# Kernel tuning notes

Measured on AMD Instinct MI355X. Metric: run time of the kernel, lower is better.

Reference implementation:

```python
import jax, jax.numpy as jnp
import numpy as np

N_NODES = 50000
N_EDGES = 800000
D = 128          # node_state_dim
H = 256          # edge hidden / message dim (= 2*D)
NH = 256         # node MLP hidden


def setup_inputs() -> dict:
    key = jax.random.key(0)
    ks = jax.random.split(key, 20)
    s = 0.05
    inp = {
        "node_states": jax.random.normal(ks[0], (N_NODES, D), jnp.float32),
        "edge_features": jax.random.normal(ks[1], (N_EDGES, 1), jnp.float32),
        "from_idx": jax.random.randint(ks[2], (N_EDGES,), 0, N_NODES, jnp.int32),
        "to_idx": jax.random.randint(ks[3], (N_EDGES,), 0, N_NODES, jnp.int32),
        # forward-direction message net: Linear(2D+1 -> H), ReLU, Linear(H -> H)
        "W1": jax.random.normal(ks[4], (2 * D + 1, H), jnp.float32) * s,
        "b1": jnp.zeros((H,), jnp.float32),
        "W2": jax.random.normal(ks[5], (H, H), jnp.float32) * s,
        "b2": jnp.zeros((H,), jnp.float32),
        # reverse-direction message net (separate params)
        "RW1": jax.random.normal(ks[6], (2 * D + 1, H), jnp.float32) * s,
        "Rb1": jnp.zeros((H,), jnp.float32),
        "RW2": jax.random.normal(ks[7], (H, H), jnp.float32) * s,
        "Rb2": jnp.zeros((H,), jnp.float32),
        # node update MLP: Linear(3D -> NH), ReLU, Linear(NH -> D)
        "Wn1": jax.random.normal(ks[8], (3 * D, NH), jnp.float32) * s,
        "bn1": jnp.zeros((NH,), jnp.float32),
        "Wn2": jax.random.normal(ks[9], (NH, D), jnp.float32) * s,
        "bn2": jnp.zeros((D,), jnp.float32),
    }
    return inp


def _mlp2(x, W1, b1, W2, b2):
    return jax.nn.relu(x @ W1 + b1) @ W2 + b2


def reference(node_states, edge_features, from_idx, to_idx,
              W1, b1, W2, b2, RW1, Rb1, RW2, Rb2, Wn1, bn1, Wn2, bn2):
    n_nodes = node_states.shape[0]
    from_states = node_states[from_idx]            # [E, D]
    to_states = node_states[to_idx]                # [E, D]

    # forward direction: messages go to to_idx
    edge_in = jnp.concatenate([from_states, to_states, edge_features], axis=-1)  # [E, 2D+1]
    msgs = _mlp2(edge_in, W1, b1, W2, b2)                                        # [E, H]
    agg = jax.ops.segment_sum(msgs, to_idx, num_segments=n_nodes)                # [N, H]

    # reverse direction: swap roles, aggregate onto from_idx
    redge_in = jnp.concatenate([to_states, from_states, edge_features], axis=-1)
    rmsgs = _mlp2(redge_in, RW1, Rb1, RW2, Rb2)
    agg = agg + jax.ops.segment_sum(rmsgs, from_idx, num_segments=n_nodes)

    # residual node update: MLP on [agg, node_states] -> [N, D]
    upd_in = jnp.concatenate([agg, node_states], axis=-1)                        # [N, 3D]
    return node_states + _mlp2(upd_in, Wn1, bn1, Wn2, bn2)
```

## Files before the change

### kernel.cpp

```cpp
#include <hip/hip_runtime.h>
#include <hip/hip_bf16.h>


typedef __bf16 bf16;
typedef __attribute__((ext_vector_type(8))) __bf16 bf16x8;
typedef __attribute__((ext_vector_type(4))) __bf16 bf16x4v;
typedef __attribute__((ext_vector_type(4))) float floatx4;
typedef __attribute__((ext_vector_type(2))) float floatx2;

#define DD 128
#define HH 256
#define CAPB 1408
#define MAXBINS 1600

__device__ __forceinline__ bf16x8 ns8(const float* __restrict__ NS, int row, int col, int N) {
    bf16x8 v;
    if (row < N) {
        float4 f0 = *(const float4*)&NS[(size_t)row * DD + col];
        float4 f1 = *(const float4*)&NS[(size_t)row * DD + col + 4];
        v[0] = (bf16)f0.x; v[1] = (bf16)f0.y; v[2] = (bf16)f0.z; v[3] = (bf16)f0.w;
        v[4] = (bf16)f1.x; v[5] = (bf16)f1.y; v[6] = (bf16)f1.z; v[7] = (bf16)f1.w;
    } else {
        v = (bf16x8)(bf16)0.0f;
    }
    return v;
}

__global__ void k_prep(const float* __restrict__ W1, const float* __restrict__ RW1,
                       const float* __restrict__ W2, const float* __restrict__ RW2,
                       const float* __restrict__ Wn1, const float* __restrict__ Wn2,
                       const float* __restrict__ b2, const float* __restrict__ Rb2,
                       bf16* __restrict__ Wt1, bf16* __restrict__ Wth,
                       bf16* __restrict__ Wt2, float* __restrict__ u,
                       float* __restrict__ ru) {
    const int b = blockIdx.x, t = threadIdx.x;
    if (b < 512) {
        int idx = b * 256 + t;
        int n = idx >> 7, k = idx & 127;
        float v;
        if (n < 256)      v = W1[k * 256 + n];
        else if (n < 512) v = W1[(128 + k) * 256 + (n - 256)];
        else if (n < 768) v = RW1[k * 256 + (n - 512)];
        else              v = RW1[(128 + k) * 256 + (n - 768)];
        Wt1[idx] = (bf16)v;
    } else if (b < 1152) {
        int k = b - 512, m = t;
        float v;
        if (k < 512) {
            const float* Wsrc = (k < 256) ? W2 : RW2;
            int i = k & 255;
            float acc = 0.f;
            for (int j = 0; j < 256; ++j) acc += Wsrc[i * 256 + j] * Wn1[j * 256 + m];
            v = acc;
        } else {
            v = Wn1[(256 + k - 512) * 256 + m];
        }
        Wth[m * 640 + k] = (bf16)v;
    } else if (b < 1280) {
        int idx = (b - 1152) * 256 + t;
        int n = idx >> 8, k = idx & 255;
        Wt2[idx] = (bf16)Wn2[k * 128 + n];
    } else {
        int m = t;
        float a = 0.f, bb = 0.f;
        for (int j = 0; j < 256; ++j) {
            float w = Wn1[j * 256 + m];
            a += b2[j] * w;
            bb += Rb2[j] * w;
        }
        u[m] = a;
        ru[m] = bb;
    }
}

__global__ __launch_bounds__(256) void k_bins(
    const int* __restrict__ from_idx, const int* __restrict__ to_idx,
    const float* __restrict__ ef, int* __restrict__ gcur,
    int2* __restrict__ binbuf, int E, int NP, int NBINS) {
    __shared__ int hist[MAXBINS];
    __shared__ int base[MAXBINS];
    const int t = threadIdx.x;
    const int NBF = NP >> 6;
    for (int i = t; i < NBINS; i += 256) hist[i] = 0;
    __syncthreads();
    const int e0 = blockIdx.x * 2048;
    int f[8], tt[8]; float w[8]; bool valid[8];
#pragma unroll
    for (int q = 0; q < 8; ++q) {
        int e = e0 + q * 256 + t;
        valid[q] = e < E;
        int ec = valid[q] ? e : 0;
        f[q] = from_idx[ec]; tt[q] = to_idx[ec]; w[q] = ef[ec];
    }
#pragma unroll
    for (int q = 0; q < 8; ++q) {
        if (valid[q]) {
            atomicAdd(&hist[tt[q] >> 6], 1);
            atomicAdd(&hist[NBF + (f[q] >> 6)], 1);
        }
    }
    __syncthreads();
    for (int i = t; i < NBINS; i += 256) {
        int h = hist[i];
        base[i] = h ? atomicAdd(&gcur[i], h) : 0;
        hist[i] = 0;
    }
    __syncthreads();
#pragma unroll
    for (int q = 0; q < 8; ++q) {
        if (valid[q]) {
            int wb = __float_as_int(w[q]);
            int b1 = tt[q] >> 6;
            int r1 = base[b1] + atomicAdd(&hist[b1], 1);
            if (r1 < CAPB)
                binbuf[(size_t)b1 * CAPB + r1] = make_int2(((tt[q] & 63) << 17) | f[q], wb);
            int b2 = NBF + (f[q] >> 6);
            int r2 = base[b2] + atomicAdd(&hist[b2], 1);
            if (r2 < CAPB)
                binbuf[(size_t)b2 * CAPB + r2] = make_int2(((f[q] & 63) << 17) | tt[q], wb);
        }
    }
}

__global__ __launch_bounds__(256) void k_proj(const float* __restrict__ NS,
                                              const bf16* __restrict__ Wt,
                                              unsigned char* __restrict__ Pn,
                                              bf16* __restrict__ Pf, int N) {
    __shared__ __align__(16) bf16 As[2][64][40];
    __shared__ __align__(16) bf16 Bs[2][64][40];
    const int tid = threadIdx.x;
    const int wv = tid >> 6, lane = tid & 63;
    const int l15 = lane & 15, quad = lane >> 4;
    const int row0 = blockIdx.y * 64, col0 = blockIdx.x * 64;
    const int srow = tid >> 2, kc = (tid & 3) * 8;
    floatx4 acc[4] = {};
    for (int k0 = 0; k0 < DD; k0 += 64) {
        bf16x8 av0 = ns8(NS, row0 + srow, k0 + kc, N);
        bf16x8 av1 = ns8(NS, row0 + srow, k0 + 32 + kc, N);
        bf16x8 bv0 = *(const bf16x8*)&Wt[(size_t)(col0 + srow) * DD + k0 + kc];
        bf16x8 bv1 = *(const bf16x8*)&Wt[(size_t)(col0 + srow) * DD + k0 + 32 + kc];
        __syncthreads();
        *(bf16x8*)&As[0][srow][kc] = av0;
        *(bf16x8*)&As[1][srow][kc] = av1;
        *(bf16x8*)&Bs[0][srow][kc] = bv0;
        *(bf16x8*)&Bs[1][srow][kc] = bv1;
        __syncthreads();
#pragma unroll
        for (int h = 0; h < 2; ++h) {
            bf16x8 bfr = *(const bf16x8*)&Bs[h][wv * 16 + l15][quad * 8];
#pragma unroll
            for (int r = 0; r < 4; ++r) {
                bf16x8 afr = *(const bf16x8*)&As[h][r * 16 + l15][quad * 8];
                acc[r] = __builtin_amdgcn_mfma_f32_16x16x32_bf16(afr, bfr, acc[r], 0, 0, 0);
            }
        }
    }
    const int ocol = col0 + wv * 16 + l15;
    const int ch = ocol & 255;
    const int half = (ocol >> 9) & 1;
    const bool isNbr = ((ocol >> 8) & 1) == 0;
#pragma unroll
    for (int r = 0; r < 4; ++r)
#pragma unroll
        for (int i = 0; i < 4; ++i) {
            int orow = row0 + r * 16 + quad * 4 + i;
            float v = acc[r][i];
            if (isNbr) {
                int pk = __builtin_amdgcn_cvt_pk_fp8_f32(v, v, 0, false);
                Pn[(size_t)orow * 512 + half * 256 + ch] = (unsigned char)(pk & 0xFF);
            } else {
                Pf[(size_t)orow * 512 + half * 256 + ch] = (bf16)v;
            }
        }
}

__global__ __launch_bounds__(256) void k_aggf(
    const unsigned char* __restrict__ Pn, const bf16* __restrict__ Pf,
    const int2* __restrict__ binbuf, const int* __restrict__ gcnt,
    const float* __restrict__ W1, const float* __restrict__ b1,
    const float* __restrict__ RW1, const float* __restrict__ Rb1,
    bf16* __restrict__ S_to, bf16* __restrict__ S_fr,
    int* __restrict__ deg, int NP) {
    __shared__ int hist[64], kstart[64], cur[64], scanbuf[64];
    __shared__ int2 srec[CAPB];
    const int b = blockIdx.x, t = threadIdx.x;
    const int NBF = NP >> 6;
    const bool rev = b >= NBF;
    const int node0 = (rev ? b - NBF : b) << 6;
    int cnt = gcnt[b]; if (cnt > CAPB) cnt = CAPB;
    const int2* bin = binbuf + (size_t)b * CAPB;
    if (t < 64) hist[t] = 0;
    __syncthreads();
    for (int i = t; i < cnt; i += 256)
        atomicAdd(&hist[((unsigned)bin[i].x) >> 17], 1);
    __syncthreads();
    if (t < 64) scanbuf[t] = hist[t];
    __syncthreads();
    for (int d = 1; d < 64; d <<= 1) {
        int v = (t < 64 && t >= d) ? scanbuf[t - d] : 0;
        __syncthreads();
        if (t < 64) scanbuf[t] += v;
        __syncthreads();
    }
    if (t < 64) { kstart[t] = scanbuf[t] - hist[t]; cur[t] = scanbuf[t] - hist[t]; }
    __syncthreads();
    for (int i = t; i < cnt; i += 256) {
        int2 r = bin[i];
        int rk = atomicAdd(&cur[((unsigned)r.x) >> 17], 1);
        srec[rk] = r;
    }
    __syncthreads();
    const int wv = t >> 6, lane = t & 63, c = lane * 4;
    const int fixoff = rev ? 256 : 0;
    const int nbroff = rev ? 256 : 0;
    const float* bb = rev ? Rb1 : b1;
    const float* wl = (rev ? RW1 : W1) + 65536;
    float4 bv = *(const float4*)&bb[c];
    float4 wv4 = *(const float4*)&wl[c];
    bf16* Sarr = rev ? S_fr : S_to;
    for (int key = wv; key < 64; key += 4) {
        int node = node0 + key;
        bf16x4v pf = *(const bf16x4v*)&Pf[(size_t)node * 512 + fixoff + c];
        float fx0 = (float)pf[0] + bv.x;
        float fx1 = (float)pf[1] + bv.y;
        float fx2 = (float)pf[2] + bv.z;
        float fx3 = (float)pf[3] + bv.w;
        int beg = kstart[key], kc2 = hist[key], end = beg + kc2;
        float a0 = 0.f, a1 = 0.f, a2 = 0.f, a3 = 0.f;
        int j = beg;
        for (; j + 4 <= end; j += 4) {
            int2 r0 = srec[j], r1 = srec[j + 1], r2 = srec[j + 2], r3 = srec[j + 3];
            int q0 = *(const int*)&Pn[(size_t)(r0.x & 0x1FFFF) * 512 + nbroff + c];
            int q1 = *(const int*)&Pn[(size_t)(r1.x & 0x1FFFF) * 512 + nbroff + c];
            int q2 = *(const int*)&Pn[(size_t)(r2.x & 0x1FFFF) * 512 + nbroff + c];
            int q3 = *(const int*)&Pn[(size_t)(r3.x & 0x1FFFF) * 512 + nbroff + c];
#pragma unroll
            for (int z = 0; z < 4; ++z) {
                int qq = z == 0 ? q0 : z == 1 ? q1 : z == 2 ? q2 : q3;
                float w = __int_as_float(z == 0 ? r0.y : z == 1 ? r1.y : z == 2 ? r2.y : r3.y);
                floatx2 lo = __builtin_amdgcn_cvt_pk_f32_fp8(qq, false);
                floatx2 hi = __builtin_amdgcn_cvt_pk_f32_fp8(qq, true);
                a0 += fmaxf(fx0 + lo.x + w * wv4.x, 0.f);
                a1 += fmaxf(fx1 + lo.y + w * wv4.y, 0.f);
                a2 += fmaxf(fx2 + hi.x + w * wv4.z, 0.f);
                a3 += fmaxf(fx3 + hi.y + w * wv4.w, 0.f);
            }
        }
        for (; j < end; ++j) {
            int2 r = srec[j];
            int qq = *(const int*)&Pn[(size_t)(r.x & 0x1FFFF) * 512 + nbroff + c];
            float w = __int_as_float(r.y);
            floatx2 lo = __builtin_amdgcn_cvt_pk_f32_fp8(qq, false);
            floatx2 hi = __builtin_amdgcn_cvt_pk_f32_fp8(qq, true);
            a0 += fmaxf(fx0 + lo.x + w * wv4.x, 0.f);
            a1 += fmaxf(fx1 + lo.y + w * wv4.y, 0.f);
            a2 += fmaxf(fx2 + hi.x + w * wv4.z, 0.f);
            a3 += fmaxf(fx3 + hi.y + w * wv4.w, 0.f);
        }
        bf16x4v o;
        o[0] = (bf16)a0; o[1] = (bf16)a1; o[2] = (bf16)a2; o[3] = (bf16)a3;
        *(bf16x4v*)&Sarr[(size_t)node * 256 + c] = o;
        if (lane == 0) deg[(rev ? NP : 0) + node] = kc2;
    }
}

__global__ __launch_bounds__(256) void k_node(
    const bf16* __restrict__ S_to, const bf16* __restrict__ S_fr,
    const float* __restrict__ NS, const bf16* __restrict__ Wth,
    const bf16* __restrict__ Wt2,
    const float* __restrict__ u, const float* __restrict__ ru,
    const float* __restrict__ bn1, const float* __restrict__ bn2,
    const int* __restrict__ deg, float* __restrict__ out, int NP, int N) {
    __shared__ __align__(16) unsigned char smem[33792];
    bf16 (*As)[40]  = (bf16(*)[40])smem;
    bf16 (*Bs)[40]  = (bf16(*)[40])(smem + 5120);
    bf16 (*Hs)[264] = (bf16(*)[264])smem;
    const int tid = threadIdx.x;
    const int wv = tid >> 6, lane = tid & 63;
    const int l15 = lane & 15, quad = lane >> 4;
    const int row0 = blockIdx.x * 64;
    const int srow = tid >> 2, kc = (tid & 3) * 8;
    floatx4 acc[4][4] = {};
    const int arow = row0 + srow;
    for (int k0 = 0; k0 < 640; k0 += 32) {
        bf16x8 av;
        if (k0 < 512) {
            const bf16* S = (k0 < 256) ? S_to : S_fr;
            av = *(const bf16x8*)&S[(size_t)arow * 256 + (k0 & 255) + kc];
        } else {
            av = ns8(NS, arow, (k0 - 512) + kc, N);
        }
        bf16x8 bv[4];
#pragma unroll
        for (int j = 0; j < 4; ++j)
            bv[j] = *(const bf16x8*)&Wth[(size_t)(srow + 64 * j) * 640 + k0 + kc];
        __syncthreads();
        *(bf16x8*)&As[srow][kc] = av;
#pragma unroll
        for (int j = 0; j < 4; ++j)
            *(bf16x8*)&Bs[srow + 64 * j][kc] = bv[j];
        __syncthreads();
#pragma unroll
        for (int s = 0; s < 4; ++s) {
            bf16x8 bfr = *(const bf16x8*)&Bs[wv * 64 + s * 16 + l15][quad * 8];
#pragma unroll
            for (int r = 0; r < 4; ++r) {
                bf16x8 afr = *(const bf16x8*)&As[r * 16 + l15][quad * 8];
                acc[s][r] = __builtin_amdgcn_mfma_f32_16x16x32_bf16(afr, bfr, acc[s][r], 0, 0, 0);
            }
        }
    }
    __syncthreads();
#pragma unroll
    for (int s = 0; s < 4; ++s) {
        int col = wv * 64 + s * 16 + l15;
        float uc = u[col], rc = ru[col], bc = bn1[col];
#pragma unroll
        for (int r = 0; r < 4; ++r)
#pragma unroll
            for (int i = 0; i < 4; ++i) {
                int row = r * 16 + quad * 4 + i;
                float v = acc[s][r][i] + (float)deg[row0 + row] * uc
                        + (float)deg[NP + row0 + row] * rc + bc;
                Hs[row][col] = (bf16)fmaxf(v, 0.f);
            }
    }
    __syncthreads();
    floatx4 acc2[2][4] = {};
    for (int k0 = 0; k0 < HH; k0 += 32) {
        bf16x8 afr[4];
#pragma unroll
        for (int r = 0; r < 4; ++r)
            afr[r] = *(const bf16x8*)&Hs[r * 16 + l15][k0 + quad * 8];
#pragma unroll
        for (int s = 0; s < 2; ++s) {
            int col = wv * 32 + s * 16 + l15;
            bf16x8 bfr = *(const bf16x8*)&Wt2[(size_t)col * HH + k0 + quad * 8];
#pragma unroll
            for (int r = 0; r < 4; ++r)
                acc2[s][r] = __builtin_amdgcn_mfma_f32_16x16x32_bf16(afr[r], bfr, acc2[s][r], 0, 0, 0);
        }
    }
#pragma unroll
    for (int s = 0; s < 2; ++s) {
        int ocol = wv * 32 + s * 16 + l15;
        float bb = bn2[ocol];
#pragma unroll
        for (int r = 0; r < 4; ++r)
#pragma unroll
            for (int i = 0; i < 4; ++i) {
                int orow = row0 + r * 16 + quad * 4 + i;
                if (orow < N)
                    out[(size_t)orow * DD + ocol] = acc2[s][r][i] + bb + NS[(size_t)orow * DD + ocol];
            }
    }
}

extern "C" void kernel_launch(void* const* d_in, const int* in_sizes, int n_in,
                              void* d_out, int out_size, void* d_ws, size_t ws_size,
                              hipStream_t stream) {
    const float* NS   = (const float*)d_in[0];
    const float* ef   = (const float*)d_in[1];
    const int* from_idx = (const int*)d_in[2];
    const int* to_idx   = (const int*)d_in[3];
    const float* W1  = (const float*)d_in[4];
    const float* b1  = (const float*)d_in[5];
    const float* W2  = (const float*)d_in[6];
    const float* b2  = (const float*)d_in[7];
    const float* RW1 = (const float*)d_in[8];
    const float* Rb1 = (const float*)d_in[9];
    const float* RW2 = (const float*)d_in[10];
    const float* Rb2 = (const float*)d_in[11];
    const float* Wn1 = (const float*)d_in[12];
    const float* bn1 = (const float*)d_in[13];
    const float* Wn2 = (const float*)d_in[14];
    const float* bn2 = (const float*)d_in[15];

    const int N  = in_sizes[0] / DD;
    const int E  = in_sizes[2];
    const int NP = ((N + 63) / 64) * 64;
    const int MB = NP / 64;
    const int NBF = NP / 64;
    const int NBINS = 2 * NBF;

    char* base = (char*)d_ws;
    size_t off_b = 0;
    auto alloc = [&](size_t b) { size_t o = off_b; off_b += (b + 255) & ~(size_t)255; return o; };
    unsigned char* Pn = (unsigned char*)(base + alloc((size_t)NP * 512));
    bf16* Pf   = (bf16*)(base + alloc((size_t)NP * 512 * 2));
    bf16* S_to = (bf16*)(base + alloc((size_t)NP * 256 * 2));
    bf16* S_fr = (bf16*)(base + alloc((size_t)NP * 256 * 2));
    int* deg   = (int*)(base + alloc((size_t)2 * NP * 4));
    int* gcur  = (int*)(base + alloc((size_t)NBINS * 4));
    int2* binbuf = (int2*)(base + alloc((size_t)NBINS * CAPB * 8));
    bf16* Wt1 = (bf16*)(base + alloc(1024 * 128 * 2));
    bf16* Wth = (bf16*)(base + alloc(256 * 640 * 2));
    bf16* Wt2 = (bf16*)(base + alloc(128 * 256 * 2));
    float* u  = (float*)(base + alloc(256 * 4));
    float* ru = (float*)(base + alloc(256 * 4));

    hipMemsetAsync(gcur, 0, (size_t)NBINS * 4, stream);

    k_prep<<<1281, 256, 0, stream>>>(W1, RW1, W2, RW2, Wn1, Wn2, b2, Rb2,
                                     Wt1, Wth, Wt2, u, ru);

    k_bins<<<(E + 2047) / 2048, 256, 0, stream>>>(from_idx, to_idx, ef, gcur,
                                                  binbuf, E, NP, NBINS);

    k_proj<<<dim3(16, MB), 256, 0, stream>>>(NS, Wt1, Pn, Pf, N);
    k_aggf<<<NBINS, 256, 0, stream>>>(Pn, Pf, binbuf, gcur, W1, b1, RW1, Rb1,
                                      S_to, S_fr, deg, NP);
    k_node<<<MB, 256, 0, stream>>>(S_to, S_fr, NS, Wth, Wt2, u, ru, bn1, bn2,
                                   deg, (float*)d_out, NP, N);
}
```

Baseline: 343.0 us.

## Merge prep, binning and projection into one front kernel; deepen aggregation and node loops

Three independent kernels (weight prep, edge binning, node projection) become one launch that splits by block index. The projection now reads W1/RW1 directly from fp32 and converts them in shared memory, so the transposed Wt1 buffer is gone. The aggregation gather loop is unrolled from 4 to 8 records to keep more loads in flight. The node kernel loads 64-wide K chunks (two halves) per barrier pair instead of 32, halving barrier count at the cost of more shared memory (51 KB), which may reduce occupancy.

New measurement: 346.1 us. About the same (+0.9%).

```diff
diff --git a/kernel.cpp b/kernel.cpp
--- a/kernel.cpp
+++ b/kernel.cpp
@@ -26,152 +26,158 @@
     return v;
 }
 
-__global__ void k_prep(const float* __restrict__ W1, const float* __restrict__ RW1,
-                       const float* __restrict__ W2, const float* __restrict__ RW2,
-                       const float* __restrict__ Wn1, const float* __restrict__ Wn2,
-                       const float* __restrict__ b2, const float* __restrict__ Rb2,
-                       bf16* __restrict__ Wt1, bf16* __restrict__ Wth,
-                       bf16* __restrict__ Wt2, float* __restrict__ u,
-                       float* __restrict__ ru) {
+__global__ __launch_bounds__(256) void k_front(
+    const float* __restrict__ NS, const int* __restrict__ from_idx,
+    const int* __restrict__ to_idx, const float* __restrict__ ef,
+    const float* __restrict__ W1, const float* __restrict__ RW1,
+    const float* __restrict__ W2, const float* __restrict__ RW2,
+    const float* __restrict__ Wn1, const float* __restrict__ Wn2,
+    const float* __restrict__ b2, const float* __restrict__ Rb2,
+    int* __restrict__ gcur, int2* __restrict__ binbuf,
+    unsigned char* __restrict__ Pn, bf16* __restrict__ Pf,
+    bf16* __restrict__ Wth, bf16* __restrict__ Wt2,
+    float* __restrict__ u, float* __restrict__ ru,
+    int E, int N, int NP, int NBINS, int BINB, int MB) {
+    __shared__ __align__(16) unsigned char smem[20608];
     const int b = blockIdx.x, t = threadIdx.x;
-    if (b < 512) {
-        int idx = b * 256 + t;
-        int n = idx >> 7, k = idx & 127;
-        float v;
-        if (n < 256)      v = W1[k * 256 + n];
-        else if (n < 512) v = W1[(128 + k) * 256 + (n - 256)];
-        else if (n < 768) v = RW1[k * 256 + (n - 512)];
-        else              v = RW1[(128 + k) * 256 + (n - 768)];
-        Wt1[idx] = (bf16)v;
-    } else if (b < 1152) {
-        int k = b - 512, m = t;
-        float v;
-        if (k < 512) {
-            const float* Wsrc = (k < 256) ? W2 : RW2;
-            int i = k & 255;
-            float acc = 0.f;
-            for (int j = 0; j < 256; ++j) acc += Wsrc[i * 256 + j] * Wn1[j * 256 + m];
-            v = acc;
+
+    if (b < BINB) {
+        int* hist = (int*)smem;
+        int* base = hist + MAXBINS;
+        const int NBF = NP >> 6;
+        for (int i = t; i < NBINS; i += 256) hist[i] = 0;
+        __syncthreads();
+        const int e0 = b * 2048;
+        int f[8], tt[8]; float w[8]; bool valid[8];
+#pragma unroll
+        for (int q = 0; q < 8; ++q) {
+            int e = e0 + q * 256 + t;
+            valid[q] = e < E;
+            int ec = valid[q] ? e : 0;
+            f[q] = from_idx[ec]; tt[q] = to_idx[ec]; w[q] = ef[ec];
+        }
+#pragma unroll
+        for (int q = 0; q < 8; ++q) {
+            if (valid[q]) {
+                atomicAdd(&hist[tt[q] >> 6], 1);
+                atomicAdd(&hist[NBF + (f[q] >> 6)], 1);
+            }
+        }
+        __syncthreads();
+        for (int i = t; i < NBINS; i += 256) {
+            int h = hist[i];
+            base[i] = h ? atomicAdd(&gcur[i], h) : 0;
+            hist[i] = 0;
+        }
+        __syncthreads();
+#pragma unroll
+        for (int q = 0; q < 8; ++q) {
+            if (valid[q]) {
+                int wb = __float_as_int(w[q]);
+                int b1 = tt[q] >> 6;
+                int r1 = base[b1] + atomicAdd(&hist[b1], 1);
+                if (r1 < CAPB)
+                    binbuf[(size_t)b1 * CAPB + r1] = make_int2(((tt[q] & 63) << 17) | f[q], wb);
+                int b2i = NBF + (f[q] >> 6);
+                int r2 = base[b2i] + atomicAdd(&hist[b2i], 1);
+                if (r2 < CAPB)
+                    binbuf[(size_t)b2i * CAPB + r2] = make_int2(((f[q] & 63) << 17) | tt[q], wb);
+            }
+        }
+        return;
+    }
+
+    if (b < BINB + 769) {
+        int bb = b - BINB;
+        if (bb < 640) {
+            int k = bb, m = t;
+            float v;
+            if (k < 512) {
+                const float* Wsrc = (k < 256) ? W2 : RW2;
+                int i = k & 255;
+                float acc = 0.f;
+                for (int j = 0; j < 256; ++j) acc += Wsrc[i * 256 + j] * Wn1[j * 256 + m];
+                v = acc;
+            } else {
+                v = Wn1[(256 + k - 512) * 256 + m];
+            }
+            Wth[m * 640 + k] = (bf16)v;
+        } else if (bb < 768) {
+            int idx = (bb - 640) * 256 + t;
+            int n = idx >> 8, k = idx & 255;
+            Wt2[idx] = (bf16)Wn2[k * 128 + n];
         } else {
-            v = Wn1[(256 + k - 512) * 256 + m];
-        }
-        Wth[m * 640 + k] = (bf16)v;
-    } else if (b < 1280) {
-        int idx = (b - 1152) * 256 + t;
-        int n = idx >> 8, k = idx & 255;
-        Wt2[idx] = (bf16)Wn2[k * 128 + n];
-    } else {
-        int m = t;
-        float a = 0.f, bb = 0.f;
-        for (int j = 0; j < 256; ++j) {
-            float w = Wn1[j * 256 + m];
-            a += b2[j] * w;
-            bb += Rb2[j] * w;
-        }
-        u[m] = a;
-        ru[m] = bb;
-    }
-}
-
-__global__ __launch_bounds__(256) void k_bins(
-    const int* __restrict__ from_idx, const int* __restrict__ to_idx,
-    const float* __restrict__ ef, int* __restrict__ gcur,
-    int2* __restrict__ binbuf, int E, int NP, int NBINS) {
-    __shared__ int hist[MAXBINS];
-    __shared__ int base[MAXBINS];
-    const int t = threadIdx.x;
-    const int NBF = NP >> 6;
-    for (int i = t; i < NBINS; i += 256) hist[i] = 0;
-    __syncthreads();
-    const int e0 = blockIdx.x * 2048;
-    int f[8], tt[8]; float w[8]; bool valid[8];
-#pragma unroll
-    for (int q = 0; q < 8; ++q) {
-        int e = e0 + q * 256 + t;
-        valid[q] = e < E;
-        int ec = valid[q] ? e : 0;
-        f[q] = from_idx[ec]; tt[q] = to_idx[ec]; w[q] = ef[ec];
-    }
-#pragma unroll
-    for (int q = 0; q < 8; ++q) {
-        if (valid[q]) {
-            atomicAdd(&hist[tt[q] >> 6], 1);
-            atomicAdd(&hist[NBF + (f[q] >> 6)], 1);
-        }
-    }
-    __syncthreads();
-    for (int i = t; i < NBINS; i += 256) {
-        int h = hist[i];
-        base[i] = h ? atomicAdd(&gcur[i], h) : 0;
-        hist[i] = 0;
-    }
-    __syncthreads();
-#pragma unroll
-    for (int q = 0; q < 8; ++q) {
-        if (valid[q]) {
-            int wb = __float_as_int(w[q]);
-            int b1 = tt[q] >> 6;
-            int r1 = base[b1] + atomicAdd(&hist[b1], 1);
-            if (r1 < CAPB)
-                binbuf[(size_t)b1 * CAPB + r1] = make_int2(((tt[q] & 63) << 17) | f[q], wb);
-            int b2 = NBF + (f[q] >> 6);
-            int r2 = base[b2] + atomicAdd(&hist[b2], 1);
-            if (r2 < CAPB)
-                binbuf[(size_t)b2 * CAPB + r2] = make_int2(((f[q] & 63) << 17) | tt[q], wb);
-        }
-    }
-}
-
-__global__ __launch_bounds__(256) void k_proj(const float* __restrict__ NS,
-                                              const bf16* __restrict__ Wt,
-                                              unsigned char* __restrict__ Pn,
-                                              bf16* __restrict__ Pf, int N) {
-    __shared__ __align__(16) bf16 As[2][64][40];
-    __shared__ __align__(16) bf16 Bs[2][64][40];
-    const int tid = threadIdx.x;
-    const int wv = tid >> 6, lane = tid & 63;
-    const int l15 = lane & 15, quad = lane >> 4;
-    const int row0 = blockIdx.y * 64, col0 = blockIdx.x * 64;
-    const int srow = tid >> 2, kc = (tid & 3) * 8;
-    floatx4 acc[4] = {};
-    for (int k0 = 0; k0 < DD; k0 += 64) {
-        bf16x8 av0 = ns8(NS, row0 + srow, k0 + kc, N);
-        bf16x8 av1 = ns8(NS, row0 + srow, k0 + 32 + kc, N);
-        bf16x8 bv0 = *(const bf16x8*)&Wt[(size_t)(col0 + srow) * DD + k0 + kc];
-        bf16x8 bv1 = *(const bf16x8*)&Wt[(size_t)(col0 + srow) * DD + k0 + 32 + kc];
-        __syncthreads();
-        *(bf16x8*)&As[0][srow][kc] = av0;
-        *(bf16x8*)&As[1][srow][kc] = av1;
-        *(bf16x8*)&Bs[0][srow][kc] = bv0;
-        *(bf16x8*)&Bs[1][srow][kc] = bv1;
-        __syncthreads();
-#pragma unroll
-        for (int h = 0; h < 2; ++h) {
-            bf16x8 bfr = *(const bf16x8*)&Bs[h][wv * 16 + l15][quad * 8];
-#pragma unroll
-            for (int r = 0; r < 4; ++r) {
-                bf16x8 afr = *(const bf16x8*)&As[h][r * 16 + l15][quad * 8];
-                acc[r] = __builtin_amdgcn_mfma_f32_16x16x32_bf16(afr, bfr, acc[r], 0, 0, 0);
-            }
-        }
-    }
-    const int ocol = col0 + wv * 16 + l15;
-    const int ch = ocol & 255;
-    const int half = (ocol >> 9) & 1;
-    const bool isNbr = ((ocol >> 8) & 1) == 0;
-#pragma unroll
-    for (int r = 0; r < 4; ++r)
-#pragma unroll
-        for (int i = 0; i < 4; ++i) {
-            int orow = row0 + r * 16 + quad * 4 + i;
-            float v = acc[r][i];
-            if (isNbr) {
-                int pk = __builtin_amdgcn_cvt_pk_fp8_f32(v, v, 0, false);
-                Pn[(size_t)orow * 512 + half * 256 + ch] = (unsigned char)(pk & 0xFF);
-            } else {
-                Pf[(size_t)orow * 512 + half * 256 + ch] = (bf16)v;
-            }
-        }
+            int m = t;
+            float a = 0.f, c2 = 0.f;
+            for (int j = 0; j < 256; ++j) {
+                float w = Wn1[j * 256 + m];
+                a += b2[j] * w;
+                c2 += Rb2[j] * w;
+            }
+            u[m] = a;
+            ru[m] = c2;
+        }
+        return;
+    }
+
+    {
+        bf16 (*As)[64][40] = (bf16(*)[64][40])smem;
+        bf16 (*Bs)[64][40] = (bf16(*)[64][40])(smem + 10240);
+        const int p = b - (BINB + 769);
+        const int col0 = (p / MB) * 64;
+        const int row0 = (p % MB) * 64;
+        const int wv = t >> 6, lane = t & 63;
+        const int l15 = lane & 15, quad = lane >> 4;
+        const int srow = t >> 2, kc = (t & 3) * 8;
+        const int cb = col0 >> 8;
+        const float* Wsrc = (cb < 2) ? W1 : RW1;
+        const int krow_off = (cb & 1) ? 128 : 0;
+        const int nb = col0 & 255;
+        const int nloc = t & 63, kq = t >> 6;
+        const int hB = kq >> 1, kk0 = (kq & 1) * 16;
+        floatx4 acc[4] = {};
+        for (int k0 = 0; k0 < DD; k0 += 64) {
+            bf16x8 av0 = ns8(NS, row0 + srow, k0 + kc, N);
+            bf16x8 av1 = ns8(NS, row0 + srow, k0 + 32 + kc, N);
+            float bvals[16];
+#pragma unroll
+            for (int j = 0; j < 16; ++j)
+                bvals[j] = Wsrc[(size_t)(krow_off + k0 + hB * 32 + kk0 + j) * 256 + nb + nloc];
+            __syncthreads();
+            *(bf16x8*)&As[0][srow][kc] = av0;
+            *(bf16x8*)&As[1][srow][kc] = av1;
+#pragma unroll
+            for (int j = 0; j < 16; ++j)
+                Bs[hB][nloc][kk0 + j] = (bf16)bvals[j];
+            __syncthreads();
+#pragma unroll
+            for (int h = 0; h < 2; ++h) {
+                bf16x8 bfr = *(const bf16x8*)&Bs[h][wv * 16 + l15][quad * 8];
+#pragma unroll
+                for (int r = 0; r < 4; ++r) {
+                    bf16x8 afr = *(const bf16x8*)&As[h][r * 16 + l15][quad * 8];
+                    acc[r] = __builtin_amdgcn_mfma_f32_16x16x32_bf16(afr, bfr, acc[r], 0, 0, 0);
+                }
+            }
+        }
+        const int ocol = col0 + wv * 16 + l15;
+        const int ch = ocol & 255;
+        const int half = (ocol >> 9) & 1;
+        const bool isNbr = ((ocol >> 8) & 1) == 0;
+#pragma unroll
+        for (int r = 0; r < 4; ++r)
+#pragma unroll
+            for (int i = 0; i < 4; ++i) {
+                int orow = row0 + r * 16 + quad * 4 + i;
+                float v = acc[r][i];
+                if (isNbr) {
+                    int pk = __builtin_amdgcn_cvt_pk_fp8_f32(v, v, 0, false);
+                    Pn[(size_t)orow * 512 + half * 256 + ch] = (unsigned char)(pk & 0xFF);
+                } else {
+                    Pf[(size_t)orow * 512 + half * 256 + ch] = (bf16)v;
+                }
+            }
+    }
 }
 
 __global__ __launch_bounds__(256) void k_aggf(
@@ -228,18 +234,18 @@
         int beg = kstart[key], kc2 = hist[key], end = beg + kc2;
         float a0 = 0.f, a1 = 0.f, a2 = 0.f, a3 = 0.f;
         int j = beg;
-        for (; j + 4 <= end; j += 4) {
-            int2 r0 = srec[j], r1 = srec[j + 1], r2 = srec[j + 2], r3 = srec[j + 3];
-            int q0 = *(const int*)&Pn[(size_t)(r0.x & 0x1FFFF) * 512 + nbroff + c];
-            int q1 = *(const int*)&Pn[(size_t)(r1.x & 0x1FFFF) * 512 + nbroff + c];
-            int q2 = *(const int*)&Pn[(size_t)(r2.x & 0x1FFFF) * 512 + nbroff + c];
-            int q3 = *(const int*)&Pn[(size_t)(r3.x & 0x1FFFF) * 512 + nbroff + c];
-#pragma unroll
-            for (int z = 0; z < 4; ++z) {
-                int qq = z == 0 ? q0 : z == 1 ? q1 : z == 2 ? q2 : q3;
-                float w = __int_as_float(z == 0 ? r0.y : z == 1 ? r1.y : z == 2 ? r2.y : r3.y);
-                floatx2 lo = __builtin_amdgcn_cvt_pk_f32_fp8(qq, false);
-                floatx2 hi = __builtin_amdgcn_cvt_pk_f32_fp8(qq, true);
+        for (; j + 8 <= end; j += 8) {
+            int2 rr[8]; int qq[8];
+#pragma unroll
+            for (int z = 0; z < 8; ++z) rr[z] = srec[j + z];
+#pragma unroll
+            for (int z = 0; z < 8; ++z)
+                qq[z] = *(const int*)&Pn[(size_t)(rr[z].x & 0x1FFFF) * 512 + nbroff + c];
+#pragma unroll
+            for (int z = 0; z < 8; ++z) {
+                float w = __int_as_float(rr[z].y);
+                floatx2 lo = __builtin_amdgcn_cvt_pk_f32_fp8(qq[z], false);
+                floatx2 hi = __builtin_amdgcn_cvt_pk_f32_fp8(qq[z], true);
                 a0 += fmaxf(fx0 + lo.x + w * wv4.x, 0.f);
                 a1 += fmaxf(fx1 + lo.y + w * wv4.y, 0.f);
                 a2 += fmaxf(fx2 + hi.x + w * wv4.z, 0.f);
@@ -271,44 +277,53 @@
     const float* __restrict__ u, const float* __restrict__ ru,
     const float* __restrict__ bn1, const float* __restrict__ bn2,
     const int* __restrict__ deg, float* __restrict__ out, int NP, int N) {
-    __shared__ __align__(16) unsigned char smem[33792];
-    bf16 (*As)[40]  = (bf16(*)[40])smem;
-    bf16 (*Bs)[40]  = (bf16(*)[40])(smem + 5120);
+    __shared__ __align__(16) unsigned char smem[51200];
+    bf16 (*As)[64][40]  = (bf16(*)[64][40])smem;
+    bf16 (*Bs)[256][40] = (bf16(*)[256][40])(smem + 10240);
     bf16 (*Hs)[264] = (bf16(*)[264])smem;
     const int tid = threadIdx.x;
     const int wv = tid >> 6, lane = tid & 63;
     const int l15 = lane & 15, quad = lane >> 4;
     const int row0 = blockIdx.x * 64;
-    const int srow = tid >> 2, kc = (tid & 3) * 8;
+    const int srow4 = tid >> 2, kc = (tid & 3) * 8;
     floatx4 acc[4][4] = {};
-    const int arow = row0 + srow;
-    for (int k0 = 0; k0 < 640; k0 += 32) {
-        bf16x8 av;
-        if (k0 < 512) {
-            const bf16* S = (k0 < 256) ? S_to : S_fr;
-            av = *(const bf16x8*)&S[(size_t)arow * 256 + (k0 & 255) + kc];
-        } else {
-            av = ns8(NS, arow, (k0 - 512) + kc, N);
-        }
-        bf16x8 bv[4];
-#pragma unroll
-        for (int j = 0; j < 4; ++j)
-            bv[j] = *(const bf16x8*)&Wth[(size_t)(srow + 64 * j) * 640 + k0 + kc];
-        __syncthreads();
-        *(bf16x8*)&As[srow][kc] = av;
-#pragma unroll
-        for (int j = 0; j < 4; ++j)
-            *(bf16x8*)&Bs[srow + 64 * j][kc] = bv[j];
-        __syncthreads();
-#pragma unroll
-        for (int s = 0; s < 4; ++s) {
-            bf16x8 bfr = *(const bf16x8*)&Bs[wv * 64 + s * 16 + l15][quad * 8];
-#pragma unroll
-            for (int r = 0; r < 4; ++r) {
-                bf16x8 afr = *(const bf16x8*)&As[r * 16 + l15][quad * 8];
-                acc[s][r] = __builtin_amdgcn_mfma_f32_16x16x32_bf16(afr, bfr, acc[s][r], 0, 0, 0);
-            }
-        }
+    const int arow = row0 + srow4;
+    auto loadA = [&](int k) -> bf16x8 {
+        if (k < 512) {
+            const bf16* S = (k < 256) ? S_to : S_fr;
+            return *(const bf16x8*)&S[(size_t)arow * 256 + (k & 255) + kc];
+        }
+        return ns8(NS, arow, (k - 512) + kc, N);
+    };
+    for (int k0 = 0; k0 < 640; k0 += 64) {
+        bf16x8 av0 = loadA(k0);
+        bf16x8 av1 = loadA(k0 + 32);
+        bf16x8 bv[2][4];
+#pragma unroll
+        for (int h = 0; h < 2; ++h)
+#pragma unroll
+            for (int j = 0; j < 4; ++j)
+                bv[h][j] = *(const bf16x8*)&Wth[(size_t)(srow4 + 64 * j) * 640 + k0 + h * 32 + kc];
+        __syncthreads();
+        *(bf16x8*)&As[0][srow4][kc] = av0;
+        *(bf16x8*)&As[1][srow4][kc] = av1;
+#pragma unroll
+        for (int h = 0; h < 2; ++h)
+#pragma unroll
+            for (int j = 0; j < 4; ++j)
+                *(bf16x8*)&Bs[h][srow4 + 64 * j][kc] = bv[h][j];
+        __syncthreads();
+#pragma unroll
+        for (int h = 0; h < 2; ++h)
+#pragma unroll
+            for (int s = 0; s < 4; ++s) {
+                bf16x8 bfr = *(const bf16x8*)&Bs[h][wv * 64 + s * 16 + l15][quad * 8];
+#pragma unroll
+                for (int r = 0; r < 4; ++r) {
+                    bf16x8 afr = *(const bf16x8*)&As[h][r * 16 + l15][quad * 8];
+                    acc[s][r] = __builtin_amdgcn_mfma_f32_16x16x32_bf16(afr, bfr, acc[s][r], 0, 0, 0);
+                }
+            }
     }
     __syncthreads();
 #pragma unroll
@@ -382,6 +397,8 @@
     const int MB = NP / 64;
     const int NBF = NP / 64;
     const int NBINS = 2 * NBF;
+    const int BINB = (E + 2047) / 2048;
+    const int FRONT = BINB + 769 + 16 * MB;
 
     char* base = (char*)d_ws;
     size_t off_b = 0;
@@ -393,7 +410,6 @@
     int* deg   = (int*)(base + alloc((size_t)2 * NP * 4));
     int* gcur  = (int*)(base + alloc((size_t)NBINS * 4));
     int2* binbuf = (int2*)(base + alloc((size_t)NBINS * CAPB * 8));
-    bf16* Wt1 = (bf16*)(base + alloc(1024 * 128 * 2));
     bf16* Wth = (bf16*)(base + alloc(256 * 640 * 2));
     bf16* Wt2 = (bf16*)(base + alloc(128 * 256 * 2));
     float* u  = (float*)(base + alloc(256 * 4));
@@ -401,13 +417,10 @@
 
     hipMemsetAsync(gcur, 0, (size_t)NBINS * 4, stream);
 
-    k_prep<<<1281, 256, 0, stream>>>(W1, RW1, W2, RW2, Wn1, Wn2, b2, Rb2,
-                                     Wt1, Wth, Wt2, u, ru);
-
-    k_bins<<<(E + 2047) / 2048, 256, 0, stream>>>(from_idx, to_idx, ef, gcur,
-                                                  binbuf, E, NP, NBINS);
-
-    k_proj<<<dim3(16, MB), 256, 0, stream>>>(NS, Wt1, Pn, Pf, N);
+    k_front<<<FRONT, 256, 0, stream>>>(NS, from_idx, to_idx, ef,
+                                       W1, RW1, W2, RW2, Wn1, Wn2, b2, Rb2,
+                                       gcur, binbuf, Pn, Pf, Wth, Wt2, u, ru,
+                                       E, N, NP, NBINS, BINB, MB);
     k_aggf<<<NBINS, 256, 0, stream>>>(Pn, Pf, binbuf, gcur, W1, b1, RW1, Rb1,
                                       S_to, S_fr, deg, NP);
     k_node<<<MB, 256, 0, stream>>>(S_to, S_fr, NS, Wth, Wt2, u, ru, bn1, bn2,
```
